# Kernel tuning notes

Measured on AMD Instinct MI355X. Metric: run time of the kernel, lower is better.

Reference implementation:

```python
import jax, jax.numpy as jnp
import numpy as np

D_MODEL = 1024
N_HEADS = 16
D_FF = 4096
EPS = 1e-6


def layernorm(x, alpha, bias):
    # torch.std uses Bessel correction (ddof=1)
    mean = jnp.mean(x, axis=-1, keepdims=True)
    std = jnp.std(x, axis=-1, keepdims=True, ddof=1)
    return alpha * (x - mean) / (std + EPS) + bias


def setup_inputs() -> dict:
    key = jax.random.key(0)
    ks = jax.random.split(key, 12)
    s = 1.0 / np.sqrt(D_MODEL)
    sf = 1.0 / np.sqrt(D_FF)
    return {
        "x": jax.random.normal(ks[0], (2, 2048, D_MODEL), jnp.float32),
        "mask": jnp.ones((2, 1, 1, 2048), jnp.int32),
        "wq": jax.random.normal(ks[1], (D_MODEL, D_MODEL), jnp.float32) * s,
        "wk": jax.random.normal(ks[2], (D_MODEL, D_MODEL), jnp.float32) * s,
        "wv": jax.random.normal(ks[3], (D_MODEL, D_MODEL), jnp.float32) * s,
        "wo": jax.random.normal(ks[4], (D_MODEL, D_MODEL), jnp.float32) * s,
        "wo_b": jnp.zeros((D_MODEL,), jnp.float32),
        "w1": jax.random.normal(ks[5], (D_MODEL, D_FF), jnp.float32) * s,
        "b1": jnp.zeros((D_FF,), jnp.float32),
        "w2": jax.random.normal(ks[6], (D_FF, D_MODEL), jnp.float32) * sf,
        "b2": jnp.zeros((D_MODEL,), jnp.float32),
        "alpha1": jnp.ones((D_MODEL,), jnp.float32),
        "bias1": jnp.zeros((D_MODEL,), jnp.float32),
        "alpha2": jnp.ones((D_MODEL,), jnp.float32),
        "bias2": jnp.zeros((D_MODEL,), jnp.float32),
    }


def reference(x, mask, wq, wk, wv, wo, wo_b, w1, b1, w2, b2,
              alpha1, bias1, alpha2, bias2):
    B, S, D = x.shape
    h, dk = N_HEADS, D_MODEL // N_HEADS
    # projections -> [B, h, S, dk]
    q = (x @ wq).reshape(B, S, h, dk).transpose(0, 2, 1, 3)
    k = (x @ wk).reshape(B, S, h, dk).transpose(0, 2, 1, 3)
    v = (x @ wv).reshape(B, S, h, dk).transpose(0, 2, 1, 3)
    scores = jnp.einsum('bhqd,bhkd->bhqk', q, k) / jnp.sqrt(jnp.float32(dk))
    scores = jnp.where(mask == 0, jnp.float32(-1e9), scores)
    attn = jax.nn.softmax(scores, axis=-1)
    ctx = jnp.einsum('bhqk,bhkd->bhqd', attn, v)
    ctx = ctx.transpose(0, 2, 1, 3).reshape(B, S, D)
    attn_out = ctx @ wo + wo_b
    x = layernorm(x + attn_out, alpha1, bias1)
    ff = jax.nn.relu(x @ w1 + b1) @ w2 + b2
    x = layernorm(x + ff, alpha2, bias2)
    return x
```

## Files before the change

### kernel.cpp

```cpp
#include <hip/hip_runtime.h>
#include <hip/hip_bf16.h>

#define D_MODEL 1024
#define N_HEADS 16
#define DK      64
#define SEQ     2048
#define BATCH   2
#define D_FF    4096
#define ROWS    (BATCH*SEQ)
#define LN_EPS  1e-6f
#define KTILE   128

typedef __hip_bfloat16 bf16;
typedef __attribute__((ext_vector_type(8))) short frag8;
typedef __attribute__((ext_vector_type(4))) float facc4;

__device__ inline float bf2f(unsigned short u){ return __uint_as_float(((unsigned)u) << 16); }
__device__ inline float toF(bf16 v){ return __bfloat162float(v); }
__device__ inline unsigned short f2bu(float f){ bf16 h = __float2bfloat16(f); return *reinterpret_cast<unsigned short*>(&h); }

__device__ inline unsigned cvtpk_bf16(float lo, float hi){
    unsigned r;
    asm("v_cvt_pk_bf16_f32 %0, %1, %2" : "=v"(r) : "v"(lo), "v"(hi));
    return r;
}

__device__ inline float ld1(const void* p, size_t idx, bool f32) {
    return f32 ? ((const float*)p)[idx] : toF(((const bf16*)p)[idx]);
}

struct U8 { unsigned short v[8]; };
__device__ inline U8 ld8bf(const void* p, size_t idx, bool f32) {
    U8 r;
    if (!f32) {
        *reinterpret_cast<uint4*>(r.v) = *reinterpret_cast<const uint4*>((const unsigned short*)p + idx);
    } else {
        const float* f = (const float*)p + idx;
        const float4 a = *reinterpret_cast<const float4*>(f);
        const float4 b = *reinterpret_cast<const float4*>(f + 4);
        r.v[0]=f2bu(a.x); r.v[1]=f2bu(a.y); r.v[2]=f2bu(a.z); r.v[3]=f2bu(a.w);
        r.v[4]=f2bu(b.x); r.v[5]=f2bu(b.y); r.v[6]=f2bu(b.z); r.v[7]=f2bu(b.w);
    }
    return r;
}

__device__ inline void ld8f(const void* p, int idx, bool f32, float* o) {
    if (!f32) {
        uint4 u = *reinterpret_cast<const uint4*>((const unsigned short*)p + idx);
        const unsigned short* us = reinterpret_cast<const unsigned short*>(&u);
        #pragma unroll
        for (int j = 0; j < 8; ++j) o[j] = bf2f(us[j]);
    } else {
        const float* f = (const float*)p + idx;
        const float4 a = *reinterpret_cast<const float4*>(f);
        const float4 b = *reinterpret_cast<const float4*>(f + 4);
        o[0]=a.x; o[1]=a.y; o[2]=a.z; o[3]=a.w;
        o[4]=b.x; o[5]=b.y; o[6]=b.z; o[7]=b.w;
    }
}

__device__ inline void gld16(const void* g, void* l) {
    __builtin_amdgcn_global_load_lds(
        reinterpret_cast<const __attribute__((address_space(1))) void*>(
            reinterpret_cast<uintptr_t>(g)),
        reinterpret_cast<__attribute__((address_space(3))) void*>(
            (unsigned int)reinterpret_cast<uintptr_t>(l)),
        16, 0, 0);
}

__global__ void probe_kernel(const void* __restrict__ xp, int* __restrict__ flag) {
    __shared__ int hit;
    if (threadIdx.x == 0) hit = 0;
    __syncthreads();
    const bf16* p = (const bf16*)xp;
    int bad = 0;
    for (int i = threadIdx.x; i < 8192; i += 256) {
        float v = fabsf(toF(p[i]));
        if (!(v <= 1e5f)) bad = 1;
    }
    if (bad) atomicOr(&hit, 1);
    __syncthreads();
    if (threadIdx.x == 0) *flag = hit;
}

__global__ __launch_bounds__(256) void xcvt_kernel(const void* __restrict__ x,
    bf16* __restrict__ out, const int* __restrict__ flagp)
{
    const bool f32 = (*flagp) != 0;
    const size_t i = ((size_t)blockIdx.x * 256 + threadIdx.x) * 8;
    U8 d = ld8bf(x, i, f32);
    *reinterpret_cast<uint4*>(out + i) = *reinterpret_cast<const uint4*>(d.v);
}

__device__ inline void ttile(const void* W, bf16* WT, int K, int N,
                             int n0, int k0, bool f32, float (*tile)[65], int t)
{
    const int lr = t >> 2;
    const int lc = (t & 3) * 16;
    if (!f32) {
        const unsigned short* src = (const unsigned short*)W + (size_t)(k0 + lr) * N + n0 + lc;
        uint4 u0 = *reinterpret_cast<const uint4*>(src);
        uint4 u1 = *reinterpret_cast<const uint4*>(src + 8);
        const unsigned short* us0 = reinterpret_cast<const unsigned short*>(&u0);
        const unsigned short* us1 = reinterpret_cast<const unsigned short*>(&u1);
        #pragma unroll
        for (int j = 0; j < 8; ++j) {
            tile[lr][lc + j]     = bf2f(us0[j]);
            tile[lr][lc + 8 + j] = bf2f(us1[j]);
        }
    } else {
        const float* src = (const float*)W + (size_t)(k0 + lr) * N + n0 + lc;
        #pragma unroll
        for (int q4 = 0; q4 < 4; ++q4) {
            const float4 f = *reinterpret_cast<const float4*>(src + 4 * q4);
            tile[lr][lc + 4*q4 + 0] = f.x;
            tile[lr][lc + 4*q4 + 1] = f.y;
            tile[lr][lc + 4*q4 + 2] = f.z;
            tile[lr][lc + 4*q4 + 3] = f.w;
        }
    }
    __syncthreads();
    unsigned short o[16];
    #pragma unroll
    for (int j = 0; j < 16; ++j) o[j] = f2bu(tile[lc + j][lr]);
    bf16* dst = WT + (size_t)(n0 + lr) * K + k0 + lc;
    *reinterpret_cast<uint4*>(dst)     = *reinterpret_cast<const uint4*>(&o[0]);
    *reinterpret_cast<uint4*>(dst + 8) = *reinterpret_cast<const uint4*>(&o[8]);
}

__global__ __launch_bounds__(256) void transpose_kernel(const void* __restrict__ W,
    bf16* __restrict__ WT, int K, int N, const int* __restrict__ flagp)
{
    __shared__ float tile[64][65];
    ttile(W, WT, K, N, blockIdx.x * 64, blockIdx.y * 64, (*flagp) != 0, tile, threadIdx.x);
}

__global__ __launch_bounds__(256) void prep_kernel(
    const void* __restrict__ x, bf16* __restrict__ Xb,
    const void* __restrict__ wq, const void* __restrict__ wk,
    const void* __restrict__ wv, const void* __restrict__ wo, bf16* __restrict__ WT4,
    const void* __restrict__ w1, const void* __restrict__ w2,
    bf16* __restrict__ W1T, bf16* __restrict__ W2T,
    const int* __restrict__ flagp)
{
    __shared__ float tile[64][65];
    const bool f32 = (*flagp) != 0;
    const int id = blockIdx.x;
    if (id < 2048) {
        const size_t i = ((size_t)id * 256 + threadIdx.x) * 8;
        U8 d = ld8bf(x, i, f32);
        *reinterpret_cast<uint4*>(Xb + i) = *reinterpret_cast<const uint4*>(d.v);
        return;
    }
    if (id < 3072) {
        const int local = id - 2048;
        const int which = local >> 8;
        const void* W = (which == 0) ? wq : (which == 1) ? wk : (which == 2) ? wv : wo;
        bf16* WT = WT4 + (size_t)which * D_MODEL * D_MODEL;
        const int rem = local & 255;
        ttile(W, WT, D_MODEL, D_MODEL, (rem & 15) * 64, (rem >> 4) * 64, f32, tile, threadIdx.x);
        return;
    }
    const int local = id - 3072;
    const int z = local >> 10, bid = local & 1023;
    const void* W = z ? w2 : w1;
    bf16* WT = z ? W2T : W1T;
    const int K = z ? D_FF : D_MODEL;
    const int N = z ? D_MODEL : D_FF;
    const int n0 = (z ? (bid & 15) : (bid & 63)) * 64;
    const int k0 = (z ? (bid >> 4) : (bid >> 6)) * 64;
    ttile(W, WT, K, N, n0, k0, f32, tile, threadIdx.x);
}

template<bool RELU, bool BIAS, int NMAT, int SPLITK>
__global__ __launch_bounds__(256) void mgemm_kernel(const bf16* __restrict__ A,
    const bf16* __restrict__ BT, const void* __restrict__ bias,
    bf16* __restrict__ C, int M, int N, int K, const int* __restrict__ flagp)
{
    const bool inF32 = (*flagp) != 0;

    __shared__ unsigned short sA[128 * 64];
    __shared__ unsigned short sB[128 * 64];

    const int gx  = gridDim.x, gy = gridDim.y;
    const int nwg = gx * gy * gridDim.z;
    const int lin = blockIdx.x + gx * (blockIdx.y + gy * blockIdx.z);
    const int rid = (lin & 7) * (nwg >> 3) + (lin >> 3);
    const int by  = rid % gy;
    const int tq  = rid / gy;
    const int bx  = tq % gx;
    const int bz  = tq / gx;

    int which = 0, colb = bx;
    if (NMAT > 1) { which = bx >> 3; colb = bx & 7; }
    const int kslice = (SPLITK > 1) ? bz : 0;
    const int Kspan  = K / SPLITK;
    const int kbase  = kslice * Kspan;
    const bf16* Bp = BT + (size_t)which * N * K;
    bf16*       Cp = C  + (size_t)which * M * N + (size_t)kslice * M * N;

    const int row0 = by * 128;
    const int col0 = colb * 128;

    const int t    = threadIdx.x;
    const int wave = t >> 6;
    const int lane = t & 63;
    const int lm   = lane & 15;
    const int q    = lane >> 4;
    const int wm   = (wave & 1) * 64;
    const int wn   = (wave >> 1) * 64;

    facc4 acc[4][4];
    #pragma unroll
    for (int i = 0; i < 4; ++i)
        #pragma unroll
        for (int j = 0; j < 4; ++j)
            acc[i][j] = (facc4){0.f, 0.f, 0.f, 0.f};

    for (int k0 = kbase; k0 < kbase + Kspan; k0 += 64) {
        __syncthreads();
        #pragma unroll
        for (int j = 0; j < 4; ++j) {
            const int ch = (wave * 4 + j) * 64 + lane;
            const int r  = ch >> 3;
            const int cs = ch & 7;
            const int c  = cs ^ (r & 7);
            gld16(A  + (size_t)(row0 + r) * K + k0 + 8 * c, &sA[(wave * 4 + j) * 512]);
            gld16(Bp + (size_t)(col0 + r) * K + k0 + 8 * c, &sB[(wave * 4 + j) * 512]);
        }
        __syncthreads();

        #pragma unroll
        for (int kk = 0; kk < 64; kk += 32) {
            const int cr = (kk >> 3) + q;
            frag8 af[4], bfr[4];
            #pragma unroll
            for (int im = 0; im < 4; ++im) {
                const int m = wm + 16 * im + lm;
                af[im] = *reinterpret_cast<const frag8*>(&sA[m * 64 + ((cr ^ (m & 7)) << 3)]);
            }
            #pragma unroll
            for (int in = 0; in < 4; ++in) {
                const int n = wn + 16 * in + lm;
                bfr[in] = *reinterpret_cast<const frag8*>(&sB[n * 64 + ((cr ^ (n & 7)) << 3)]);
            }
            #pragma unroll
            for (int im = 0; im < 4; ++im)
                #pragma unroll
                for (int in = 0; in < 4; ++in)
                    acc[im][in] = __builtin_amdgcn_mfma_f32_16x16x32_bf16(af[im], bfr[in], acc[im][in], 0, 0, 0);
        }
    }

    if (NMAT > 1 && which == 2) {
        #pragma unroll
        for (int in = 0; in < 4; ++in) {
            const int col = col0 + wn + 16*in + lm;
            const int hh = col >> 6, dd = col & 63;
            #pragma unroll
            for (int im = 0; im < 4; ++im) {
                const int rowb = row0 + wm + 16*im + 4*q;
                const int bb = rowb >> 11, ss = rowb & 2047;
                union { uint2 v; unsigned u[2]; } ov;
                ov.u[0] = cvtpk_bf16(acc[im][in][0], acc[im][in][1]);
                ov.u[1] = cvtpk_bf16(acc[im][in][2], acc[im][in][3]);
                *reinterpret_cast<uint2*>(Cp + ((size_t)((bb * 16 + hh) * 64 + dd)) * 2048 + ss) = ov.v;
            }
        }
        return;
    }

    #pragma unroll
    for (int in = 0; in < 4; ++in) {
        const int col = col0 + wn + 16*in + lm;
        float bv = 0.f;
        if (BIAS && kslice == 0) bv = ld1(bias, col, inF32);
        #pragma unroll
        for (int im = 0; im < 4; ++im) {
            #pragma unroll
            for (int r = 0; r < 4; ++r) {
                const int row = row0 + wm + 16*im + 4*q + r;
                float v = acc[im][in][r] + bv;
                if (RELU) v = fmaxf(v, 0.f);
                Cp[(size_t)row * N + col] = __float2bfloat16(v);
            }
        }
    }
}

__global__ __launch_bounds__(256, 2) void fattn_kernel(
    const bf16* __restrict__ Qg, const bf16* __restrict__ Kg,
    const bf16* __restrict__ VTg, const int* __restrict__ mask,
    bf16* __restrict__ ctx)
{
    __shared__ unsigned short sK[2][128 * 64];
    __shared__ unsigned short sV[2][64 * 128];
    __shared__ __align__(16) float madd[SEQ];

    const int t    = threadIdx.x;
    const int lin  = blockIdx.x + 16 * (blockIdx.y + 16 * blockIdx.z);
    const int rid  = (lin & 7) * 64 + (lin >> 3);
    const int qt   = rid & 15;
    const int h    = (rid >> 4) & 15;
    const int b    = rid >> 8;
    const int q0   = qt * 128;
    const int bh   = b * N_HEADS + h;
    const int wave = t >> 6;
    const int lane = t & 63;
    const int lm   = lane & 15;
    const int qd   = lane >> 4;
    const bool qo  = (qd & 1) != 0;

    const float SCL = 0.18033688011112042f;

    auto stage = [&](int bi, int kt) {
        const int k0 = kt * KTILE;
        #pragma unroll
        for (int j = 0; j < 4; ++j) {
            const int ch = (wave * 4 + j) * 64 + lane;
            const int rK = ch >> 3, cK = (ch & 7) ^ (rK & 7);
            gld16(Kg + ((size_t)(b * SEQ + k0 + rK)) * D_MODEL + h * DK + 8 * cK,
                  &sK[bi][(wave * 4 + j) * 512]);
            const int rV = ch >> 4, cV = (ch & 15) ^ (rV & 15);
            gld16(VTg + ((size_t)(bh * DK + rV)) * SEQ + k0 + 8 * cV,
                  &sV[bi][(wave * 4 + j) * 512]);
        }
    };

    stage(0, 0);
    #pragma unroll
    for (int i = 0; i < SEQ / (256 * 4); ++i) {
        const int idx = (i * 256 + t) * 4;
        const int4 mv = *reinterpret_cast<const int4*>(&mask[b * SEQ + idx]);
        madd[idx + 0] = (mv.x == 0) ? -1.442695e9f : 0.f;
        madd[idx + 1] = (mv.y == 0) ? -1.442695e9f : 0.f;
        madd[idx + 2] = (mv.z == 0) ? -1.442695e9f : 0.f;
        madd[idx + 3] = (mv.w == 0) ? -1.442695e9f : 0.f;
    }

    frag8 qf[2][2];
    #pragma unroll
    for (int s = 0; s < 2; ++s) {
        const bf16* qsrc = Qg + ((size_t)(b * SEQ + q0 + 32 * wave + 16 * s + lm)) * D_MODEL + h * DK;
        qf[s][0] = *reinterpret_cast<const frag8*>(qsrc + 8 * qd);
        qf[s][1] = *reinterpret_cast<const frag8*>(qsrc + 32 + 8 * qd);
    }

    facc4 accO[2][4];
    #pragma unroll
    for (int s = 0; s < 2; ++s)
        #pragma unroll
        for (int in = 0; in < 4; ++in) accO[s][in] = (facc4){0.f, 0.f, 0.f, 0.f};
    float m_r[2] = {-1e30f, -1e30f}, l_r[2] = {0.f, 0.f};

    for (int kt = 0; kt < SEQ / KTILE; ++kt) {
        const int cur = kt & 1;
        const int k0  = kt * KTILE;
        __syncthreads();
        if (kt + 1 < SEQ / KTILE) stage(cur ^ 1, kt + 1);

        facc4 accST[2][8];
        #pragma unroll
        for (int s = 0; s < 2; ++s)
            #pragma unroll
            for (int i = 0; i < 8; ++i) accST[s][i] = (facc4){0.f, 0.f, 0.f, 0.f};
        __builtin_amdgcn_s_setprio(1);
        #pragma unroll
        for (int i = 0; i < 8; ++i) {
            #pragma unroll
            for (int s2 = 0; s2 < 2; ++s2) {
                const int cr = 4 * s2 + qd;
                frag8 kf = *reinterpret_cast<const frag8*>(
                    &sK[cur][(16 * i + lm) * 64 + ((cr ^ (lm & 7)) << 3)]);
                accST[0][i] = __builtin_amdgcn_mfma_f32_16x16x32_bf16(kf, qf[0][s2], accST[0][i], 0, 0, 0);
                accST[1][i] = __builtin_amdgcn_mfma_f32_16x16x32_bf16(kf, qf[1][s2], accST[1][i], 0, 0, 0);
            }
        }
        __builtin_amdgcn_s_setprio(0);

        facc4 vmx[2];
        #pragma unroll
        for (int s = 0; s < 2; ++s) vmx[s] = (facc4){-1e30f, -1e30f, -1e30f, -1e30f};
        #pragma unroll
        for (int i = 0; i < 8; ++i) {
            const facc4 mv = *reinterpret_cast<const facc4*>(&madd[k0 + 16 * i + 4 * qd]);
            #pragma unroll
            for (int s = 0; s < 2; ++s) {
                #pragma unroll
                for (int r = 0; r < 4; ++r) {
                    accST[s][i][r] = fmaf(accST[s][i][r], SCL, mv[r]);
                    vmx[s][r] = fmaxf(vmx[s][r], accST[s][i][r]);
                }
            }
        }
        float mn[2], alpha[2] = {1.f, 1.f};
        bool resc[2];
        #pragma unroll
        for (int s = 0; s < 2; ++s) {
            const float mloc = fmaxf(fmaxf(vmx[s][0], vmx[s][1]), fmaxf(vmx[s][2], vmx[s][3]));
            const bool skip = __all(mloc - m_r[s] <= 11.54f) != 0;
            resc[s] = !skip;
            if (skip) {
                mn[s] = m_r[s];
            } else {
                float m0 = mloc;
                m0 = fmaxf(m0, __shfl_xor(m0, 16));
                m0 = fmaxf(m0, __shfl_xor(m0, 32));
                mn[s] = fmaxf(m_r[s], m0);
                alpha[s] = __builtin_amdgcn_exp2f(m_r[s] - mn[s]);
                m_r[s] = mn[s];
            }
        }

        unsigned up[2][8][2];
        facc4 ps4[2];
        #pragma unroll
        for (int s = 0; s < 2; ++s) ps4[s] = (facc4){0.f, 0.f, 0.f, 0.f};
        #pragma unroll
        for (int s = 0; s < 2; ++s) {
            #pragma unroll
            for (int i = 0; i < 8; ++i) {
                const float p0 = __builtin_amdgcn_exp2f(accST[s][i][0] - mn[s]);
                const float p1 = __builtin_amdgcn_exp2f(accST[s][i][1] - mn[s]);
                const float p2 = __builtin_amdgcn_exp2f(accST[s][i][2] - mn[s]);
                const float p3 = __builtin_amdgcn_exp2f(accST[s][i][3] - mn[s]);
                ps4[s][0] += p0; ps4[s][1] += p1; ps4[s][2] += p2; ps4[s][3] += p3;
                up[s][i][0] = cvtpk_bf16(p0, p1);
                up[s][i][1] = cvtpk_bf16(p2, p3);
            }
        }
        #pragma unroll
        for (int s = 0; s < 2; ++s) {
            float ps = (ps4[s][0] + ps4[s][1]) + (ps4[s][2] + ps4[s][3]);
            ps += __shfl_xor(ps, 16);
            ps += __shfl_xor(ps, 32);
            if (resc[s]) {
                l_r[s] = l_r[s] * alpha[s] + ps;
                #pragma unroll
                for (int in = 0; in < 4; ++in)
                    #pragma unroll
                    for (int r = 0; r < 4; ++r) accO[s][in][r] *= alpha[s];
            } else {
                l_r[s] += ps;
            }
        }

        __builtin_amdgcn_s_setprio(1);
        #pragma unroll
        for (int c = 0; c < 4; ++c) {
            union { frag8 f; unsigned u[4]; } pf0_, pf1_;
            #pragma unroll
            for (int s = 0; s < 2; ++s) {
                unsigned a0 = up[s][2*c][0],     a1 = up[s][2*c][1];
                unsigned b0 = up[s][2*c + 1][0], b1 = up[s][2*c + 1][1];
                asm("v_permlane32_swap_b32 %0, %1" : "+v"(a0), "+v"(b0));
                asm("v_permlane32_swap_b32 %0, %1" : "+v"(a1), "+v"(b1));
                const unsigned t0 = qo ? a0 : b0;
                const unsigned t1 = qo ? a1 : b1;
                const unsigned r0 = __shfl_xor(t0, 16);
                const unsigned r1 = __shfl_xor(t1, 16);
                unsigned u0 = qo ? r0 : a0;
                unsigned u1 = qo ? r1 : a1;
                unsigned u2 = qo ? b0 : r0;
                unsigned u3 = qo ? b1 : r1;
                if (s == 0) { pf0_.u[0]=u0; pf0_.u[1]=u1; pf0_.u[2]=u2; pf0_.u[3]=u3; }
                else        { pf1_.u[0]=u0; pf1_.u[1]=u1; pf1_.u[2]=u2; pf1_.u[3]=u3; }
            }
            #pragma unroll
            for (int in = 0; in < 4; ++in) {
                const int cr = 4 * c + qd;
                frag8 vf = *reinterpret_cast<const frag8*>(
                    &sV[cur][(16 * in + lm) * 128 + ((cr ^ lm) << 3)]);
                accO[0][in] = __builtin_amdgcn_mfma_f32_16x16x32_bf16(vf, pf0_.f, accO[0][in], 0, 0, 0);
                accO[1][in] = __builtin_amdgcn_mfma_f32_16x16x32_bf16(vf, pf1_.f, accO[1][in], 0, 0, 0);
            }
        }
        __builtin_amdgcn_s_setprio(0);
    }

    #pragma unroll
    for (int s = 0; s < 2; ++s) {
        const float invl = 1.f / l_r[s];
        bf16* crow = ctx + ((size_t)(b * SEQ + q0 + 32 * wave + 16 * s + lm)) * D_MODEL + h * DK;
        #pragma unroll
        for (int in = 0; in < 4; ++in) {
            union { uint2 v; unsigned u[2]; } ov;
            ov.u[0] = cvtpk_bf16(accO[s][in][0] * invl, accO[s][in][1] * invl);
            ov.u[1] = cvtpk_bf16(accO[s][in][2] * invl, accO[s][in][3] * invl);
            *reinterpret_cast<uint2*>(crow + 16 * in + 4 * qd) = ov.v;
        }
    }
}

template<bool BASE_WS, bool OUT_WS>
__global__ __launch_bounds__(128) void ln_kernel(const void* __restrict__ base,
    const bf16* __restrict__ addv, const bf16* __restrict__ addv2,
    const void* __restrict__ alpha, const void* __restrict__ bias,
    void* __restrict__ outp, const int* __restrict__ flagp)
{
    const bool inF32 = (*flagp) != 0;
    __shared__ float red[2];
    __shared__ float red2[2];
    const int row = blockIdx.x, t = threadIdx.x;
    const size_t off = (size_t)row * D_MODEL + t * 8;

    float v[8];
    {
        const U8 bz = ld8bf(base, off, BASE_WS ? false : inF32);
        uint4 a1 = *reinterpret_cast<const uint4*>(addv + off);
        const unsigned short* a1s = reinterpret_cast<const unsigned short*>(&a1);
        #pragma unroll
        for (int j = 0; j < 8; ++j) v[j] = bf2f(bz.v[j]) + bf2f(a1s[j]);
        if (addv2) {
            uint4 a2 = *reinterpret_cast<const uint4*>(addv2 + off);
            const unsigned short* a2s = reinterpret_cast<const unsigned short*>(&a2);
            #pragma unroll
            for (int j = 0; j < 8; ++j) v[j] += bf2f(a2s[j]);
        }
    }

    float s = ((v[0]+v[1]) + (v[2]+v[3])) + ((v[4]+v[5]) + (v[6]+v[7]));
    #pragma unroll
    for (int o = 1; o < 64; o <<= 1) s += __shfl_xor(s, o);
    if ((t & 63) == 0) red[t >> 6] = s;
    __syncthreads();
    const float mean = (red[0] + red[1]) * (1.f / (float)D_MODEL);

    float sq = 0.f;
    #pragma unroll
    for (int j = 0; j < 8; ++j) { const float d = v[j] - mean; sq += d * d; }
    #pragma unroll
    for (int o = 1; o < 64; o <<= 1) sq += __shfl_xor(sq, o);
    if ((t & 63) == 0) red2[t >> 6] = sq;
    __syncthreads();
    const float var = (red2[0] + red2[1]) * (1.f / (float)(D_MODEL - 1));
    const float inv = 1.f / (sqrtf(var) + LN_EPS);

    float av[8], bv[8];
    ld8f(alpha, t * 8, inF32, av);
    ld8f(bias,  t * 8, inF32, bv);
    float y[8];
    #pragma unroll
    for (int j = 0; j < 8; ++j)
        y[j] = av[j] * (v[j] - mean) * inv + bv[j];

    if (OUT_WS || !inF32) {
        union { uint4 u; unsigned w[4]; } o_;
        o_.w[0] = cvtpk_bf16(y[0], y[1]);
        o_.w[1] = cvtpk_bf16(y[2], y[3]);
        o_.w[2] = cvtpk_bf16(y[4], y[5]);
        o_.w[3] = cvtpk_bf16(y[6], y[7]);
        *reinterpret_cast<uint4*>((bf16*)outp + off) = o_.u;
    } else {
        float* op = (float*)outp + off;
        const float4 f0 = {y[0], y[1], y[2], y[3]};
        const float4 f1 = {y[4], y[5], y[6], y[7]};
        *reinterpret_cast<float4*>(op)     = f0;
        *reinterpret_cast<float4*>(op + 4) = f1;
    }
}

extern "C" void kernel_launch(void* const* d_in, const int* in_sizes, int n_in,
                              void* d_out, int out_size, void* d_ws, size_t ws_size,
                              hipStream_t stream)
{
    const void* x    = d_in[0];
    const int*  mask = (const int*)d_in[1];
    const void* wq   = d_in[2];
    const void* wk   = d_in[3];
    const void* wv   = d_in[4];
    const void* wo   = d_in[5];
    const void* wo_b = d_in[6];
    const void* w1   = d_in[7];
    const void* b1   = d_in[8];
    const void* w2   = d_in[9];
    const void* b2   = d_in[10];
    const void* al1  = d_in[11];
    const void* bi1  = d_in[12];
    const void* al2  = d_in[13];
    const void* bi2  = d_in[14];

    const size_t MB = 1024 * 1024;
    char* ws = (char*)d_ws;
    const bool BIG = ws_size >= 64 * MB + 4096;
    if (!BIG && ws_size < 56 * MB + 4096) return;

    if (BIG) {
        bf16* Qb   = (bf16*)(ws + 0 * MB);
        bf16* Kb   = (bf16*)(ws + 8 * MB);
        bf16* VTb  = (bf16*)(ws + 16 * MB);
        bf16* Xb   = (bf16*)(ws + 24 * MB);
        bf16* WT4  = (bf16*)(ws + 32 * MB);
        bf16* WOT  = WT4 + (size_t)3 * D_MODEL * D_MODEL;
        bf16* W1T  = (bf16*)(ws + 40 * MB);
        bf16* W2T  = (bf16*)(ws + 48 * MB);
        bf16* CTXb = (bf16*)(ws + 56 * MB);
        bf16* ATT0 = (bf16*)(ws + 0 * MB);
        bf16* ATT1 = (bf16*)(ws + 8 * MB);
        bf16* X1b  = (bf16*)(ws + 56 * MB);
        bf16* FFb  = (bf16*)(ws + 0 * MB);
        bf16* X20  = (bf16*)(ws + 32 * MB);
        bf16* X21  = (bf16*)(ws + 40 * MB);
        int*  flagp = (int*)(ws + 64 * MB);

        probe_kernel<<<1, 256, 0, stream>>>(x, flagp);
        prep_kernel<<<dim3(5120), 256, 0, stream>>>(x, Xb, wq, wk, wv, wo, WT4,
                                                    w1, w2, W1T, W2T, flagp);

        mgemm_kernel<false, false, 3, 1><<<dim3(24, 32), 256, 0, stream>>>(
            Xb, WT4, nullptr, Qb, ROWS, D_MODEL, D_MODEL, flagp);

        fattn_kernel<<<dim3(SEQ / 128, N_HEADS, BATCH), 256, 0, stream>>>(Qb, Kb, VTb, mask, CTXb);

        mgemm_kernel<false, true, 1, 2><<<dim3(8, 32, 2), 256, 0, stream>>>(
            CTXb, WOT, wo_b, ATT0, ROWS, D_MODEL, D_MODEL, flagp);
        ln_kernel<false, true><<<ROWS, 128, 0, stream>>>(x, ATT0, ATT1, al1, bi1, X1b, flagp);

        mgemm_kernel<true, true, 1, 1><<<dim3(32, 32), 256, 0, stream>>>(
            X1b, W1T, b1, FFb, ROWS, D_FF, D_MODEL, flagp);

        mgemm_kernel<false, true, 1, 2><<<dim3(8, 32, 2), 256, 0, stream>>>(
            FFb, W2T, b2, X20, ROWS, D_MODEL, D_FF, flagp);
        ln_kernel<true, false><<<ROWS, 128, 0, stream>>>(X1b, X20, X21, al2, bi2, d_out, flagp);
    } else {
        bf16* Qb    = (bf16*)(ws + 0 * MB);
        bf16* Kb    = (bf16*)(ws + 8 * MB);
        bf16* VTb   = (bf16*)(ws + 16 * MB);
        bf16* Xb    = (bf16*)(ws + 24 * MB);
        bf16* WQKVT = (bf16*)(ws + 32 * MB);
        bf16* CTXb  = (bf16*)(ws + 32 * MB);
        bf16* W2T   = (bf16*)(ws + 32 * MB);
        bf16* WOT   = (bf16*)(ws + 0 * MB);
        bf16* ATT0  = (bf16*)(ws + 48 * MB);
        bf16* W1T   = (bf16*)(ws + 48 * MB);
        bf16* X20   = (bf16*)(ws + 48 * MB);
        bf16* X1b   = (bf16*)(ws + 40 * MB);
        bf16* FFb   = (bf16*)(ws + 0 * MB);
        int*  flagp = (int*)(ws + 56 * MB);

        probe_kernel<<<1, 256, 0, stream>>>(x, flagp);
        xcvt_kernel<<<dim3(ROWS * D_MODEL / 2048), 256, 0, stream>>>(x, Xb, flagp);

        transpose_kernel<<<dim3(16, 16), 256, 0, stream>>>(wq, WQKVT,           D_MODEL, D_MODEL, flagp);
        transpose_kernel<<<dim3(16, 16), 256, 0, stream>>>(wk, WQKVT + 1048576, D_MODEL, D_MODEL, flagp);
        transpose_kernel<<<dim3(16, 16), 256, 0, stream>>>(wv, WQKVT + 2097152, D_MODEL, D_MODEL, flagp);

        mgemm_kernel<false, false, 3, 1><<<dim3(24, 32), 256, 0, stream>>>(
            Xb, WQKVT, nullptr, Qb, ROWS, D_MODEL, D_MODEL, flagp);

        fattn_kernel<<<dim3(SEQ / 128, N_HEADS, BATCH), 256, 0, stream>>>(Qb, Kb, VTb, mask, CTXb);

        transpose_kernel<<<dim3(16, 16), 256, 0, stream>>>(wo, WOT, D_MODEL, D_MODEL, flagp);
        mgemm_kernel<false, true, 1, 1><<<dim3(8, 32), 256, 0, stream>>>(
            CTXb, WOT, wo_b, ATT0, ROWS, D_MODEL, D_MODEL, flagp);
        ln_kernel<false, true><<<ROWS, 128, 0, stream>>>(x, ATT0, nullptr, al1, bi1, X1b, flagp);

        transpose_kernel<<<dim3(64, 16), 256, 0, stream>>>(w1, W1T, D_MODEL, D_FF, flagp);
        mgemm_kernel<true, true, 1, 1><<<dim3(32, 32), 256, 0, stream>>>(
            X1b, W1T, b1, FFb, ROWS, D_FF, D_MODEL, flagp);

        transpose_kernel<<<dim3(16, 64), 256, 0, stream>>>(w2, W2T, D_FF, D_MODEL, flagp);
        mgemm_kernel<false, true, 1, 1><<<dim3(8, 32), 256, 0, stream>>>(
            FFb, W2T, b2, X20, ROWS, D_MODEL, D_FF, flagp);
        ln_kernel<true, false><<<ROWS, 128, 0, stream>>>(X1b, X20, nullptr, al2, bi2, d_out, flagp);
    }
}
```

Before: 363.5 us.

## Use a 256x256-tile, 512-thread GEMM kernel for the FFN up-projection

Adds a new GEMM kernel that computes 256x256 output tiles with 8 waves, each owning a 128x64 sub-tile. It uses double-buffered, XOR-swizzled LDS staging with a K step of 64. The kernel replaces the 128x128 mgemm for the x@W1+b1, ReLU GEMM in both code paths. Larger tiles raise arithmetic intensity and cut global/LDS reloads. The cost is 128 KB of LDS per block, which likely allows only one block per CU, and the 256-block grid is close to the CU count, so wave quantization and occupancy may suffer.

```diff
diff --git a/kernel.cpp b/kernel.cpp
--- a/kernel.cpp
+++ b/kernel.cpp
@@ -283,6 +283,115 @@
                 float v = acc[im][in][r] + bv;
                 if (RELU) v = fmaxf(v, 0.f);
                 Cp[(size_t)row * N + col] = __float2bfloat16(v);
+            }
+        }
+    }
+}
+
+template<bool RELU, bool BIAS>
+__global__ __launch_bounds__(512, 2) void gemm256_kernel(const bf16* __restrict__ A,
+    const bf16* __restrict__ BT, const void* __restrict__ bias,
+    bf16* __restrict__ C, int M, int N, int K, const int* __restrict__ flagp)
+{
+    const bool inF32 = (*flagp) != 0;
+    __shared__ __align__(16) unsigned short sA[2][256 * 64];
+    __shared__ __align__(16) unsigned short sB[2][256 * 64];
+
+    const int gx = gridDim.x, gy = gridDim.y;
+    const int nwg = gx * gy;
+    const int lin = blockIdx.x + gx * blockIdx.y;
+    const int rid = (lin & 7) * (nwg >> 3) + (lin >> 3);
+    const int by = rid % gy;
+    const int bx = rid / gy;
+
+    const int row0 = by * 256;
+    const int col0 = bx * 256;
+
+    const int t    = threadIdx.x;
+    const int wave = t >> 6;
+    const int lane = t & 63;
+    const int lm   = lane & 15;
+    const int q    = lane >> 4;
+    const int wm   = (wave >> 2) * 128;
+    const int wn   = (wave & 3) * 64;
+
+    const int NK = K >> 6;
+
+    auto stage = [&](int bi, int kt) {
+        const int k0 = kt << 6;
+        #pragma unroll
+        for (int j = 0; j < 4; ++j) {
+            const int ch = j * 512 + t;
+            const int r  = ch >> 3;
+            const int c  = (ch & 7) ^ (r & 7);
+            gld16(A  + (size_t)(row0 + r) * K + k0 + 8 * c, &sA[bi][ch * 8]);
+            gld16(BT + (size_t)(col0 + r) * K + k0 + 8 * c, &sB[bi][ch * 8]);
+        }
+    };
+
+    facc4 acc[8][4];
+    #pragma unroll
+    for (int i = 0; i < 8; ++i)
+        #pragma unroll
+        for (int j = 0; j < 4; ++j)
+            acc[i][j] = (facc4){0.f, 0.f, 0.f, 0.f};
+
+    stage(0, 0);
+    stage(1, 1);
+    asm volatile("s_waitcnt vmcnt(8)" ::: "memory");
+    __builtin_amdgcn_s_barrier();
+
+    for (int kt = 0; kt < NK; ++kt) {
+        const int cur = kt & 1;
+
+        __builtin_amdgcn_s_setprio(1);
+        #pragma unroll
+        for (int kk = 0; kk < 64; kk += 32) {
+            const int cr = (kk >> 3) + q;
+            frag8 af[8], bfr[4];
+            #pragma unroll
+            for (int im = 0; im < 8; ++im) {
+                const int m = wm + 16 * im + lm;
+                af[im] = *reinterpret_cast<const frag8*>(&sA[cur][m * 64 + ((cr ^ (m & 7)) << 3)]);
+            }
+            #pragma unroll
+            for (int in = 0; in < 4; ++in) {
+                const int n = wn + 16 * in + lm;
+                bfr[in] = *reinterpret_cast<const frag8*>(&sB[cur][n * 64 + ((cr ^ (n & 7)) << 3)]);
+            }
+            #pragma unroll
+            for (int im = 0; im < 8; ++im)
+                #pragma unroll
+                for (int in = 0; in < 4; ++in)
+                    acc[im][in] = __builtin_amdgcn_mfma_f32_16x16x32_bf16(af[im], bfr[in], acc[im][in], 0, 0, 0);
+        }
+        __builtin_amdgcn_s_setprio(0);
+
+        asm volatile("s_waitcnt lgkmcnt(0)" ::: "memory");
+        __builtin_amdgcn_s_barrier();
+
+        if (kt + 2 < NK) {
+            stage(cur, kt + 2);
+            asm volatile("s_waitcnt vmcnt(8)" ::: "memory");
+        } else {
+            asm volatile("s_waitcnt vmcnt(0)" ::: "memory");
+        }
+        __builtin_amdgcn_s_barrier();
+    }
+
+    #pragma unroll
+    for (int in = 0; in < 4; ++in) {
+        const int col = col0 + wn + 16*in + lm;
+        float bv = 0.f;
+        if (BIAS) bv = ld1(bias, col, inF32);
+        #pragma unroll
+        for (int im = 0; im < 8; ++im) {
+            #pragma unroll
+            for (int r = 0; r < 4; ++r) {
+                const int row = row0 + wm + 16*im + 4*q + r;
+                float v = acc[im][in][r] + bv;
+                if (RELU) v = fmaxf(v, 0.f);
+                C[(size_t)row * N + col] = __float2bfloat16(v);
             }
         }
     }
@@ -616,7 +725,7 @@
             CTXb, WOT, wo_b, ATT0, ROWS, D_MODEL, D_MODEL, flagp);
         ln_kernel<false, true><<<ROWS, 128, 0, stream>>>(x, ATT0, ATT1, al1, bi1, X1b, flagp);
 
-        mgemm_kernel<true, true, 1, 1><<<dim3(32, 32), 256, 0, stream>>>(
+        gemm256_kernel<true, true><<<dim3(16, 16), 512, 0, stream>>>(
             X1b, W1T, b1, FFb, ROWS, D_FF, D_MODEL, flagp);
 
         mgemm_kernel<false, true, 1, 2><<<dim3(8, 32, 2), 256, 0, stream>>>(
@@ -656,7 +765,7 @@
         ln_kernel<false, true><<<ROWS, 128, 0, stream>>>(x, ATT0, nullptr, al1, bi1, X1b, flagp);
 
         transpose_kernel<<<dim3(64, 16), 256, 0, stream>>>(w1, W1T, D_MODEL, D_FF, flagp);
-        mgemm_kernel<true, true, 1, 1><<<dim3(32, 32), 256, 0, stream>>>(
+        gemm256_kernel<true, true><<<dim3(16, 16), 512, 0, stream>>>(
             X1b, W1T, b1, FFb, ROWS, D_FF, D_MODEL, flagp);
 
         transpose_kernel<<<dim3(16, 64), 256, 0, stream>>>(w2, W2T, D_FF, D_MODEL, flagp);
```

Measured after the change: 356.5 us. No clear change (-1.9%).
